# Optimization experiments

Hardware: AMD Instinct MI355X
Metric: run time of the kernel (lower is better)

Reference implementation:

```python
import jax, jax.numpy as jnp
import numpy as np

N = 50000      # nodes in batched graph
E = 800000     # directed edges
F_IN = 64      # node_feature_dim
F_E = 16       # edge_feature_dim
H = 4          # heads
C = 64         # hidden_dim per head
HC = H * C     # 256


def setup_inputs() -> dict:
    key = jax.random.key(0)
    ks = jax.random.split(key, 26)
    rn = lambda k, s, scale=0.1: jax.random.normal(k, s, dtype=jnp.float32) * scale
    inp = {}
    inp["x"] = rn(ks[0], (N, F_IN), 1.0)
    inp["edge_src"] = jax.random.randint(ks[1], (E,), 0, N)
    inp["edge_dst"] = jax.random.randint(ks[2], (E,), 0, N)
    inp["edge_attr"] = rn(ks[3], (E, F_E), 1.0)
    # GATConv layer 1 params
    inp["W1"] = rn(ks[4], (F_IN, HC))
    inp["atts1"] = rn(ks[5], (H, C))
    inp["attd1"] = rn(ks[6], (H, C))
    inp["We1"] = rn(ks[7], (F_E, HC))
    inp["atte1"] = rn(ks[8], (H, C))
    inp["b1"] = jnp.zeros((HC,), jnp.float32)
    inp["g1"] = jnp.ones((HC,), jnp.float32)
    inp["be1"] = jnp.zeros((HC,), jnp.float32)
    # GATConv layer 2 params
    inp["W2"] = rn(ks[9], (HC, HC))
    inp["atts2"] = rn(ks[10], (H, C))
    inp["attd2"] = rn(ks[11], (H, C))
    inp["We2"] = rn(ks[12], (F_E, HC))
    inp["atte2"] = rn(ks[13], (H, C))
    inp["b2"] = jnp.zeros((HC,), jnp.float32)
    inp["g2"] = jnp.ones((HC,), jnp.float32)
    inp["be2"] = jnp.zeros((HC,), jnp.float32)
    # output head
    inp["Wout"] = rn(ks[14], (HC, 1))
    inp["bout"] = jnp.zeros((1,), jnp.float32)
    return inp


def _gat_layer(x, src, dst, eattr, W, att_s, att_d, We, att_e, b):
    """PyG GATConv (concat=True, add_self_loops with fill_value='mean', eval so no dropout)."""
    n = x.shape[0]
    e = src.shape[0]
    # self-loop edge attr = mean of incoming edge attrs per node (0 if none)
    deg = jax.ops.segment_sum(jnp.ones((e,), x.dtype), dst, num_segments=n)
    loop_attr = jax.ops.segment_sum(eattr, dst, num_segments=n) / jnp.maximum(deg, 1.0)[:, None]
    loop = jnp.arange(n)
    src2 = jnp.concatenate([src, loop])
    dst2 = jnp.concatenate([dst, loop])
    ea2 = jnp.concatenate([eattr, loop_attr], axis=0)
    xs = (x @ W).reshape(n, H, C)                          # [N,H,C]
    a_s = jnp.einsum('nhc,hc->nh', xs, att_s)              # [N,H]
    a_d = jnp.einsum('nhc,hc->nh', xs, att_d)
    ee = (ea2 @ We).reshape(-1, H, C)                      # [E+N,H,C]
    a_e = jnp.einsum('ehc,hc->eh', ee, att_e)
    logits = jax.nn.leaky_relu(a_s[src2] + a_d[dst2] + a_e, 0.2)  # [E+N,H]
    m = jax.ops.segment_max(logits, dst2, num_segments=n)
    p = jnp.exp(logits - m[dst2])
    denom = jax.ops.segment_sum(p, dst2, num_segments=n)[dst2] + 1e-16
    alpha = p / denom                                      # segment softmax per dst node
    out = jax.ops.segment_sum(xs[src2] * alpha[:, :, None], dst2, num_segments=n)
    return out.reshape(n, HC) + b


def _bn_relu(x, g, b):
    # BatchNorm1d in training mode (batch statistics), eps=1e-5
    mu = x.mean(axis=0)
    var = ((x - mu) ** 2).mean(axis=0)
    return jax.nn.relu(g * (x - mu) * jax.lax.rsqrt(var + 1e-5) + b)


def reference(x, edge_src, edge_dst, edge_attr,
              W1, atts1, attd1, We1, atte1, b1, g1, be1,
              W2, atts2, attd2, We2, atte2, b2, g2, be2,
              Wout, bout):
    h = _gat_layer(x, edge_src, edge_dst, edge_attr, W1, atts1, attd1, We1, atte1, b1)
    h = _bn_relu(h, g1, be1)
    h = _gat_layer(h, edge_src, edge_dst, edge_attr, W2, atts2, attd2, We2, atte2, b2)
    h = _bn_relu(h, g2, be2)
    return h @ Wout + bout
```

## Files before the change

### kernel.cpp

```cpp
#include <hip/hip_runtime.h>
#include <hip/hip_bf16.h>
#include <stdint.h>

#define NNODES 50000
#define NEDGES 800000
#define HC 256

typedef unsigned short u16;
typedef __attribute__((ext_vector_type(8))) short bf16x8;
typedef __attribute__((ext_vector_type(4))) float f32x4;

__device__ __forceinline__ float b2f(u16 v) {
    return __uint_as_float(((unsigned)v) << 16);
}
__device__ __forceinline__ u16 f2b(float f) {
    unsigned u = __float_as_uint(f);
    u += 0x7fff + ((u >> 16) & 1);
    return (u16)(u >> 16);
}

__device__ __constant__ int dPO[19] = {0,16384,16640,16896,20992,21248,21504,21760,22016,
                                       87552,87808,88064,92160,92416,92672,92928,93184,93440,93441};
static const int hPO[19] = {0,16384,16640,16896,20992,21248,21504,21760,22016,
                            87552,87808,88064,92160,92416,92672,92928,93184,93440,93441};
#define TOTP 93441

__global__ void zero_init(unsigned* __restrict__ p, long nwords) {
    long i = (long)blockIdx.x * blockDim.x + threadIdx.x;
    long stride = (long)gridDim.x * blockDim.x;
    for (; i < nwords; i += stride) p[i] = 0u;
}

__global__ void detect_dtype(const unsigned* __restrict__ xbits, int* __restrict__ flag) {
    __shared__ int cnt;
    if (threadIdx.x == 0) cnt = 0;
    __syncthreads();
    int sane = 0;
    for (int i = threadIdx.x; i < 1024; i += 256) {
        unsigned lo = xbits[i] & 0xffffu;
        int e = (int)((lo >> 7) & 0xff);
        if (e >= 117 && e <= 133) sane++;
    }
    atomicAdd(&cnt, sane);
    __syncthreads();
    if (threadIdx.x == 0) *flag = (cnt >= 512) ? 1 : 0;
}

__global__ void cvt_bf16(const void* __restrict__ src, u16* __restrict__ dst, int n,
                         const int* __restrict__ flag) {
    int isbf16 = *flag;
    long no = (long)n >> 3;
    long i = (long)blockIdx.x * 256 + threadIdx.x;
    long stride = (long)gridDim.x * 256;
    if (isbf16) {
        const uint4* s = (const uint4*)src;
        uint4* d = (uint4*)dst;
        for (; i < no; i += stride) d[i] = s[i];
    } else {
        const float4* s = (const float4*)src;
        uint4* d = (uint4*)dst;
        for (; i < no; i += stride) {
            float4 a = s[i * 2], b = s[i * 2 + 1];
            uint4 o;
            o.x = (unsigned)f2b(a.x) | ((unsigned)f2b(a.y) << 16);
            o.y = (unsigned)f2b(a.z) | ((unsigned)f2b(a.w) << 16);
            o.z = (unsigned)f2b(b.x) | ((unsigned)f2b(b.y) << 16);
            o.w = (unsigned)f2b(b.z) | ((unsigned)f2b(b.w) << 16);
            d[i] = o;
        }
    }
}

struct Ptrs18 { const void* s[18]; };
__global__ void cvt_params(Ptrs18 p, u16* __restrict__ dst, const int* __restrict__ flag) {
    int i = blockIdx.x * 256 + threadIdx.x;
    if (i >= TOTP) return;
    int isbf16 = *flag;
    int idx = 0;
    #pragma unroll
    for (int j = 1; j < 18; j++) idx += (i >= dPO[j]) ? 1 : 0;
    int rel = i - dPO[idx];
    dst[i] = isbf16 ? ((const u16*)p.s[idx])[rel] : f2b(((const float*)p.s[idx])[rel]);
}

__global__ void proj_weight(const u16* __restrict__ W, const u16* __restrict__ att,
                            float* __restrict__ out, int R) {
    int i = blockIdx.x * 256 + threadIdx.x;
    if (i >= R * 4) return;
    int f = i >> 2, h = i & 3;
    float s = 0.f;
    for (int c = 0; c < 64; c++)
        s += b2f(W[f * 256 + h * 64 + c]) * b2f(att[h * 64 + c]);
    out[i] = s;
}

__global__ void proj_weight2(const u16* __restrict__ W, const u16* __restrict__ atta,
                             const u16* __restrict__ attb,
                             float* __restrict__ outa, float* __restrict__ outb, int R) {
    int i = blockIdx.x * 256 + threadIdx.x;
    if (i >= R * 4) return;
    int f = i >> 2, h = i & 3;
    float sa = 0.f, sb = 0.f;
    for (int c = 0; c < 64; c++) {
        float w = b2f(W[f * 256 + h * 64 + c]);
        sa += w * b2f(atta[h * 64 + c]);
        sb += w * b2f(attb[h * 64 + c]);
    }
    outa[i] = sa;
    outb[i] = sb;
}

__global__ void transpose_w(const u16* __restrict__ W, u16* __restrict__ WT, int K) {
    int i = blockIdx.x * 256 + threadIdx.x;
    if (i >= K * 256) return;
    int k = i / 256, c = i % 256;
    WT[c * K + k] = W[i];
}

__global__ void edge_deg(const int* __restrict__ edst, int* __restrict__ deg) {
    int e = blockIdx.x * 256 + threadIdx.x;
    if (e >= NEDGES) return;
    atomicAdd(&deg[edst[e]], 1);
}

__global__ void block_sum(const int* __restrict__ deg, int* __restrict__ bsums, int n) {
    __shared__ int lds[256];
    int i = blockIdx.x * 256 + threadIdx.x;
    lds[threadIdx.x] = (i < n) ? deg[i] : 0;
    __syncthreads();
    for (int s = 128; s; s >>= 1) {
        if (threadIdx.x < s) lds[threadIdx.x] += lds[threadIdx.x + s];
        __syncthreads();
    }
    if (threadIdx.x == 0) bsums[blockIdx.x] = lds[0];
}

__global__ void scan_bsums(const int* __restrict__ bsums, int* __restrict__ boffs, int nb) {
    __shared__ int lds[256];
    int t = threadIdx.x;
    int v = (t < nb) ? bsums[t] : 0;
    lds[t] = v;
    __syncthreads();
    for (int s = 1; s < 256; s <<= 1) {
        int u = (t >= s) ? lds[t - s] : 0;
        __syncthreads();
        lds[t] += u;
        __syncthreads();
    }
    boffs[t] = lds[t] - v;
}

__global__ void write_offsets(const int* __restrict__ deg, const int* __restrict__ boffs,
                              int* __restrict__ off, int* __restrict__ cursor, int n) {
    __shared__ int lds[256];
    int t = threadIdx.x;
    int i = blockIdx.x * 256 + t;
    int v = (i < n) ? deg[i] : 0;
    lds[t] = v;
    __syncthreads();
    for (int s = 1; s < 256; s <<= 1) {
        int u = (t >= s) ? lds[t - s] : 0;
        __syncthreads();
        lds[t] += u;
        __syncthreads();
    }
    int exc = lds[t] - v + boffs[blockIdx.x];
    if (i < n) { off[i] = exc; cursor[i] = exc; }
}

__global__ __launch_bounds__(256) void edge_stage(
    const void* __restrict__ eattr_raw, const int* __restrict__ flag,
    const int* __restrict__ esrc, const int* __restrict__ edst,
    const float* __restrict__ ve1, const float* __restrict__ ve2,
    int* __restrict__ cursor, uint4* __restrict__ rec) {
    int e = blockIdx.x * 256 + threadIdx.x;
    if (e >= NEDGES) return;
    float a[16];
    if (*flag) {
        const u16* s = (const u16*)eattr_raw + (long)e * 16;
        const uint4* q = (const uint4*)s;
        uint4 q0 = q[0], q1 = q[1];
        unsigned w0[8] = {q0.x, q0.y, q0.z, q0.w, q1.x, q1.y, q1.z, q1.w};
        #pragma unroll
        for (int j = 0; j < 8; j++) {
            a[2 * j] = b2f((u16)(w0[j] & 0xffff));
            a[2 * j + 1] = b2f((u16)(w0[j] >> 16));
        }
    } else {
        const float* s = (const float*)eattr_raw + (long)e * 16;
        #pragma unroll
        for (int j = 0; j < 16; j += 4) {
            float4 q = *(const float4*)(s + j);
            a[j] = q.x; a[j + 1] = q.y; a[j + 2] = q.z; a[j + 3] = q.w;
        }
    }
    float s1[4], s2[4];
    #pragma unroll
    for (int h = 0; h < 4; h++) {
        float t1 = 0.f, t2 = 0.f;
        #pragma unroll
        for (int f = 0; f < 16; f++) {
            t1 += a[f] * ve1[f * 4 + h];
            t2 += a[f] * ve2[f * 4 + h];
        }
        s1[h] = t1;
        s2[h] = t2;
    }
    unsigned a1lo = (unsigned)f2b(s1[0]) | ((unsigned)f2b(s1[1]) << 16);
    unsigned a1hi = (unsigned)f2b(s1[2]) | ((unsigned)f2b(s1[3]) << 16);
    unsigned a2lo = (unsigned)f2b(s2[0]) | ((unsigned)f2b(s2[1]) << 16);
    unsigned a2hi = (unsigned)f2b(s2[2]) | ((unsigned)f2b(s2[3]) << 16);
    int d = edst[e];
    int p = atomicAdd(&cursor[d], 1);
    unsigned src = (unsigned)esrc[e];
    rec[(long)p * 2 + 0] = make_uint4(src, a1lo, a1hi, 0u);
    rec[(long)p * 2 + 1] = make_uint4(src, a2lo, a2hi, 0u);
}

__global__ void bn_coef(const float* __restrict__ stats, const u16* __restrict__ g,
                        const u16* __restrict__ be, float* __restrict__ coef) {
    int c = threadIdx.x;
    float mu = stats[c] * (1.0f / NNODES);
    float var = stats[256 + c] * (1.0f / NNODES) - mu * mu;
    var = fmaxf(var, 0.f);
    float rs = rsqrtf(var + 1e-5f);
    float sc = b2f(g[c]) * rs;
    coef[c] = sc;
    coef[256 + c] = b2f(be[c]) - sc * mu;
}

__device__ __forceinline__ void gload_lds16(const u16* g, u16* l) {
    __builtin_amdgcn_global_load_lds(
        (const __attribute__((address_space(1))) unsigned*)g,
        (__attribute__((address_space(3))) unsigned*)l, 16, 0, 0);
}

template <int K, bool BN>
__global__ __launch_bounds__(256) void gemm_tile(const u16* __restrict__ A,
                                                 const u16* __restrict__ WT,
                                                 const float* __restrict__ coef,
                                                 u16* __restrict__ out) {
    __shared__ u16 As[128 * 32];
    __shared__ u16 Bs[128 * 32];
    int tid = threadIdx.x;
    int wave = tid >> 6, lane = tid & 63;
    int wr = wave >> 1, wc = wave & 1;
    int quad = lane >> 4, l15 = lane & 15;
    long row0 = (long)(blockIdx.x >> 1) * 128;
    int col0 = (blockIdx.x & 1) * 128;
    int srow = lane >> 2;
    int soct = (lane & 3) * 8;
    f32x4 acc[4][4] = {};
    for (int kk = 0; kk < K; kk += 32) {
        #pragma unroll
        for (int sub = 0; sub < 2; sub++) {
            int rr = wave * 32 + sub * 16;
            long gr = row0 + rr + srow;
            if (gr >= NNODES) gr = NNODES - 1;
            gload_lds16(A + gr * K + kk + soct, &As[rr * 32]);
            gload_lds16(WT + (long)(col0 + rr + srow) * K + kk + soct, &Bs[rr * 32]);
        }
        __syncthreads();
        bf16x8 av[4], bv[4];
        #pragma unroll
        for (int m = 0; m < 4; m++)
            av[m] = *(const bf16x8*)&As[(wr * 64 + m * 16 + l15) * 32 + quad * 8];
        if (BN) {
            int kb = kk + quad * 8;
            float4 sc0 = *(const float4*)(coef + kb);
            float4 sc1 = *(const float4*)(coef + kb + 4);
            float4 sh0 = *(const float4*)(coef + 256 + kb);
            float4 sh1 = *(const float4*)(coef + 256 + kb + 4);
            float scl[8] = {sc0.x, sc0.y, sc0.z, sc0.w, sc1.x, sc1.y, sc1.z, sc1.w};
            float shf[8] = {sh0.x, sh0.y, sh0.z, sh0.w, sh1.x, sh1.y, sh1.z, sh1.w};
            #pragma unroll
            for (int m = 0; m < 4; m++) {
                #pragma unroll
                for (int j = 0; j < 8; j++) {
                    float v = b2f((u16)av[m][j]);
                    v = fmaxf(v * scl[j] + shf[j], 0.f);
                    av[m][j] = (short)f2b(v);
                }
            }
        }
        #pragma unroll
        for (int n = 0; n < 4; n++)
            bv[n] = *(const bf16x8*)&Bs[(wc * 64 + n * 16 + l15) * 32 + quad * 8];
        #pragma unroll
        for (int m = 0; m < 4; m++)
            #pragma unroll
            for (int n = 0; n < 4; n++)
                acc[m][n] = __builtin_amdgcn_mfma_f32_16x16x32_bf16(av[m], bv[n],
                                                                    acc[m][n], 0, 0, 0);
        __syncthreads();
    }
    #pragma unroll
    for (int m = 0; m < 4; m++) {
        #pragma unroll
        for (int j = 0; j < 4; j++) {
            long r = row0 + wr * 64 + m * 16 + quad * 4 + j;
            if (r < NNODES) {
                u16* op = out + r * HC + col0 + wc * 64 + l15;
                #pragma unroll
                for (int n = 0; n < 4; n++) op[n * 16] = f2b(acc[m][n][j]);
            }
        }
    }
}

template <int K, bool BN>
__global__ __launch_bounds__(256) void proj_att(const u16* __restrict__ X,
                                                const float* __restrict__ coef,
                                                const float* __restrict__ us,
                                                const float* __restrict__ ud,
                                                float* __restrict__ as_, float* __restrict__ ad_) {
    int gw = (blockIdx.x * 256 + threadIdx.x) >> 6;
    int lane = threadIdx.x & 63;
    int node, f0;
    if (K == 64) {
        node = gw * 4 + (lane >> 4);
        f0 = (lane & 15) * 4;
    } else {
        node = gw;
        f0 = lane * 4;
    }
    if (node >= NNODES) return;
    uint2 v = *(const uint2*)(X + (long)node * K + f0);
    float xv[4] = {b2f((u16)(v.x & 0xffffu)), b2f((u16)(v.x >> 16)),
                   b2f((u16)(v.y & 0xffffu)), b2f((u16)(v.y >> 16))};
    float pas[4] = {0.f, 0.f, 0.f, 0.f}, pad[4] = {0.f, 0.f, 0.f, 0.f};
    #pragma unroll
    for (int j = 0; j < 4; j++) {
        int f = f0 + j;
        float x = xv[j];
        if (BN) x = fmaxf(x * coef[f] + coef[256 + f], 0.f);
        #pragma unroll
        for (int h = 0; h < 4; h++) {
            pas[h] += x * us[f * 4 + h];
            pad[h] += x * ud[f * 4 + h];
        }
    }
    const int omax = (K == 64) ? 8 : 32;
    #pragma unroll
    for (int h = 0; h < 4; h++) {
        for (int o = omax; o; o >>= 1) {
            pas[h] += __shfl_xor(pas[h], o);
            pad[h] += __shfl_xor(pad[h], o);
        }
    }
    bool wr = (K == 64) ? ((lane & 15) == 0) : (lane == 0);
    if (wr) {
        #pragma unroll
        for (int h = 0; h < 4; h++) {
            as_[node * 4 + h] = pas[h];
            ad_[node * 4 + h] = pad[h];
        }
    }
}

__global__ __launch_bounds__(256) void gat_fused(
    const u16* __restrict__ xs, const float* __restrict__ as_, const float* __restrict__ ad_,
    const uint4* __restrict__ rec, int layer,
    const int* __restrict__ off, const int* __restrict__ deg,
    const u16* __restrict__ bias, u16* __restrict__ out) {
    __shared__ int s_lds[4][64];
    __shared__ float w_lds[4][64][4];
    int wid = (blockIdx.x * 256 + threadIdx.x) >> 6;
    if (wid >= NNODES) return;
    int wave = threadIdx.x >> 6;
    int lane = threadIdx.x & 63;
    int d = wid;
    int st = off[d], dg = deg[d];
    int slot = lane >> 2, h = lane & 3;
    float adv = ad_[d * 4 + h];
    float m = -1e30f, s = 0.f, sae = 0.f;
    const uint4* rbase = rec + (long)st * 2 + layer;

    if (dg <= 64) {
        for (int i = slot; i < dg; i += 16) {
            uint4 r4 = rbase[(long)i * 2];
            int src = (int)r4.x;
            unsigned wsel = (h & 2) ? r4.z : r4.y;
            float aev = b2f((u16)((h & 1) ? (wsel >> 16) : (wsel & 0xffffu)));
            float t = as_[src * 4 + h] + adv + aev;
            float lg = (t > 0.f) ? t : 0.2f * t;
            if (h == 0) s_lds[wave][i] = src;
            w_lds[wave][i][h] = lg;
            sae += aev;
            float mn = fmaxf(m, lg);
            s = s * __expf(m - mn) + __expf(lg - mn);
            m = mn;
        }
        #pragma unroll
        for (int o = 4; o < 64; o <<= 1) {
            float mo = __shfl_xor(m, o), so = __shfl_xor(s, o), ao = __shfl_xor(sae, o);
            float mn = fmaxf(m, mo);
            s = s * __expf(m - mn) + so * __expf(mo - mn);
            m = mn;
            sae += ao;
        }
        float invs, wself;
        {
            float asv = as_[d * 4 + h];
            float l0 = asv + adv + sae / fmaxf((float)dg, 1.f);
            l0 = (l0 > 0.f) ? l0 : 0.2f * l0;
            float mn = fmaxf(m, l0);
            s = s * __expf(m - mn) + __expf(l0 - mn);
            m = mn;
            invs = 1.f / s;
            wself = __expf(l0 - mn) * invs;
        }
        for (int i = slot; i < dg; i += 16)
            w_lds[wave][i][h] = __expf(w_lds[wave][i][h] - m) * invs;

        int cg = lane & 31, half = lane >> 5;
        int ch8 = cg * 8;
        int h2 = cg >> 3;
        float ws2 = __shfl(wself, h2);
        const u16* xbase = xs + ch8;
        float a0, a1, a2, a3, a4, a5, a6, a7;
        {
            uint4 v = *(const uint4*)(xbase + (long)d * HC);
            float wsf = half ? 0.f : ws2;
            a0 = wsf * b2f((u16)(v.x & 0xffffu)); a1 = wsf * b2f((u16)(v.x >> 16));
            a2 = wsf * b2f((u16)(v.y & 0xffffu)); a3 = wsf * b2f((u16)(v.y >> 16));
            a4 = wsf * b2f((u16)(v.z & 0xffffu)); a5 = wsf * b2f((u16)(v.z >> 16));
            a6 = wsf * b2f((u16)(v.w & 0xffffu)); a7 = wsf * b2f((u16)(v.w >> 16));
        }
        int i = half;
        for (; i + 6 < dg; i += 8) {
            float wA = w_lds[wave][i][h2];     int sA = s_lds[wave][i];
            float wB = w_lds[wave][i + 2][h2]; int sB = s_lds[wave][i + 2];
            float wC = w_lds[wave][i + 4][h2]; int sC = s_lds[wave][i + 4];
            float wD = w_lds[wave][i + 6][h2]; int sD = s_lds[wave][i + 6];
            uint4 vA = *(const uint4*)(xbase + (long)sA * HC);
            uint4 vB = *(const uint4*)(xbase + (long)sB * HC);
            uint4 vC = *(const uint4*)(xbase + (long)sC * HC);
            uint4 vD = *(const uint4*)(xbase + (long)sD * HC);
            a0 += wA * b2f((u16)(vA.x & 0xffffu)) + wB * b2f((u16)(vB.x & 0xffffu))
                + wC * b2f((u16)(vC.x & 0xffffu)) + wD * b2f((u16)(vD.x & 0xffffu));
            a1 += wA * b2f((u16)(vA.x >> 16))     + wB * b2f((u16)(vB.x >> 16))
                + wC * b2f((u16)(vC.x >> 16))     + wD * b2f((u16)(vD.x >> 16));
            a2 += wA * b2f((u16)(vA.y & 0xffffu)) + wB * b2f((u16)(vB.y & 0xffffu))
                + wC * b2f((u16)(vC.y & 0xffffu)) + wD * b2f((u16)(vD.y & 0xffffu));
            a3 += wA * b2f((u16)(vA.y >> 16))     + wB * b2f((u16)(vB.y >> 16))
                + wC * b2f((u16)(vC.y >> 16))     + wD * b2f((u16)(vD.y >> 16));
            a4 += wA * b2f((u16)(vA.z & 0xffffu)) + wB * b2f((u16)(vB.z & 0xffffu))
                + wC * b2f((u16)(vC.z & 0xffffu)) + wD * b2f((u16)(vD.z & 0xffffu));
            a5 += wA * b2f((u16)(vA.z >> 16))     + wB * b2f((u16)(vB.z >> 16))
                + wC * b2f((u16)(vC.z >> 16))     + wD * b2f((u16)(vD.z >> 16));
            a6 += wA * b2f((u16)(vA.w & 0xffffu)) + wB * b2f((u16)(vB.w & 0xffffu))
                + wC * b2f((u16)(vC.w & 0xffffu)) + wD * b2f((u16)(vD.w & 0xffffu));
            a7 += wA * b2f((u16)(vA.w >> 16))     + wB * b2f((u16)(vB.w >> 16))
                + wC * b2f((u16)(vC.w >> 16))     + wD * b2f((u16)(vD.w >> 16));
        }
        for (; i < dg; i += 2) {
            float wA = w_lds[wave][i][h2]; int sA = s_lds[wave][i];
            uint4 vA = *(const uint4*)(xbase + (long)sA * HC);
            a0 += wA * b2f((u16)(vA.x & 0xffffu)); a1 += wA * b2f((u16)(vA.x >> 16));
            a2 += wA * b2f((u16)(vA.y & 0xffffu)); a3 += wA * b2f((u16)(vA.y >> 16));
            a4 += wA * b2f((u16)(vA.z & 0xffffu)); a5 += wA * b2f((u16)(vA.z >> 16));
            a6 += wA * b2f((u16)(vA.w & 0xffffu)); a7 += wA * b2f((u16)(vA.w >> 16));
        }
        a0 += __shfl_xor(a0, 32); a1 += __shfl_xor(a1, 32);
        a2 += __shfl_xor(a2, 32); a3 += __shfl_xor(a3, 32);
        a4 += __shfl_xor(a4, 32); a5 += __shfl_xor(a5, 32);
        a6 += __shfl_xor(a6, 32); a7 += __shfl_xor(a7, 32);
        if (half == 0) {
            uint4 bv = *(const uint4*)(bias + ch8);
            a0 += b2f((u16)(bv.x & 0xffffu)); a1 += b2f((u16)(bv.x >> 16));
            a2 += b2f((u16)(bv.y & 0xffffu)); a3 += b2f((u16)(bv.y >> 16));
            a4 += b2f((u16)(bv.z & 0xffffu)); a5 += b2f((u16)(bv.z >> 16));
            a6 += b2f((u16)(bv.w & 0xffffu)); a7 += b2f((u16)(bv.w >> 16));
            uint4 ov;
            ov.x = (unsigned)f2b(a0) | ((unsigned)f2b(a1) << 16);
            ov.y = (unsigned)f2b(a2) | ((unsigned)f2b(a3) << 16);
            ov.z = (unsigned)f2b(a4) | ((unsigned)f2b(a5) << 16);
            ov.w = (unsigned)f2b(a6) | ((unsigned)f2b(a7) << 16);
            *(uint4*)(out + (long)d * HC + ch8) = ov;
        }
        return;
    }

    for (int base = 0; base < dg; base += 16) {
        int i = base + slot;
        float lg = -1e30f, aev = 0.f, w = 0.f;
        if (i < dg) {
            uint4 r4 = rbase[(long)i * 2];
            int src = (int)r4.x;
            unsigned wsel = (h & 2) ? r4.z : r4.y;
            aev = b2f((u16)((h & 1) ? (wsel >> 16) : (wsel & 0xffffu)));
            float t = as_[src * 4 + h] + adv + aev;
            lg = (t > 0.f) ? t : 0.2f * t;
        }
        sae += aev;
        float mn = fmaxf(m, lg);
        if (i < dg) w = __expf(lg - mn);
        s = s * __expf(m - mn) + w;
        m = mn;
    }
    #pragma unroll
    for (int o = 4; o < 64; o <<= 1) {
        float mo = __shfl_xor(m, o), so = __shfl_xor(s, o), ao = __shfl_xor(sae, o);
        float mn = fmaxf(m, mo);
        s = s * __expf(m - mn) + so * __expf(mo - mn);
        m = mn;
        sae += ao;
    }
    float invs, wself;
    {
        float asv = as_[d * 4 + h];
        float l0 = asv + adv + sae / fmaxf((float)dg, 1.f);
        l0 = (l0 > 0.f) ? l0 : 0.2f * l0;
        float mn = fmaxf(m, l0);
        s = s * __expf(m - mn) + __expf(l0 - mn);
        m = mn;
        invs = 1.f / s;
        wself = __expf(l0 - mn) * invs;
    }
    int h2 = lane >> 4;
    float m2 = __shfl(m, h2);
    float is2 = __shfl(invs, h2);
    float ws2 = __shfl(wself, h2);
    float adv2 = __shfl(adv, h2);
    int cb = lane * 4;
    float a0, a1, a2, a3;
    {
        uint2 v = *(const uint2*)(xs + (long)d * HC + cb);
        a0 = ws2 * b2f((u16)(v.x & 0xffffu)); a1 = ws2 * b2f((u16)(v.x >> 16));
        a2 = ws2 * b2f((u16)(v.y & 0xffffu)); a3 = ws2 * b2f((u16)(v.y >> 16));
    }
    int slot16 = lane & 15;
    int lhi = lane & 48;
    for (int base = 0; base < dg; base += 16) {
        int cnt = min(16, dg - base);
        float wv = 0.f;
        int srcl = 0;
        if (slot16 < cnt) {
            uint4 r4 = rbase[(long)(base + slot16) * 2];
            srcl = (int)r4.x;
            unsigned wsel = (h2 & 2) ? r4.z : r4.y;
            float aev = b2f((u16)((h2 & 1) ? (wsel >> 16) : (wsel & 0xffffu)));
            float t = as_[srcl * 4 + h2] + adv2 + aev;
            t = (t > 0.f) ? t : 0.2f * t;
            wv = __expf(t - m2) * is2;
        }
        for (int j = 0; j < cnt; j++) {
            float w0 = __shfl(wv, lhi | j);
            int s0 = __shfl(srcl, j);
            uint2 v0 = *(const uint2*)(xs + (long)s0 * HC + cb);
            a0 += w0 * b2f((u16)(v0.x & 0xffffu));
            a1 += w0 * b2f((u16)(v0.x >> 16));
            a2 += w0 * b2f((u16)(v0.y & 0xffffu));
            a3 += w0 * b2f((u16)(v0.y >> 16));
        }
    }
    u16 o0 = f2b(a0 + b2f(bias[cb + 0]));
    u16 o1 = f2b(a1 + b2f(bias[cb + 1]));
    u16 o2 = f2b(a2 + b2f(bias[cb + 2]));
    u16 o3 = f2b(a3 + b2f(bias[cb + 3]));
    uint2 ov;
    ov.x = (unsigned)o0 | ((unsigned)o1 << 16);
    ov.y = (unsigned)o2 | ((unsigned)o3 << 16);
    *(uint2*)(out + (long)d * HC + cb) = ov;
}

__global__ __launch_bounds__(256) void bn_stats(const u16* __restrict__ h,
                                                float* __restrict__ stats) {
    __shared__ float lsum[256], lsq[256];
    int t = threadIdx.x;
    int p = t & 127;
    int ro = t >> 7;
    float s0 = 0.f, q0 = 0.f, s1 = 0.f, q1 = 0.f;
    for (int r = blockIdx.x * 2 + ro; r < NNODES; r += gridDim.x * 2) {
        unsigned v = *(const unsigned*)(h + (long)r * HC + 2 * p);
        float lo = b2f((u16)(v & 0xffffu)), hi = b2f((u16)(v >> 16));
        s0 += lo; q0 += lo * lo;
        s1 += hi; q1 += hi * hi;
    }
    if (ro == 1) {
        lsum[2 * p] = s0; lsum[2 * p + 1] = s1;
        lsq[2 * p] = q0;  lsq[2 * p + 1] = q1;
    }
    __syncthreads();
    if (ro == 0) {
        atomicAdd(&stats[2 * p],           s0 + lsum[2 * p]);
        atomicAdd(&stats[2 * p + 1],       s1 + lsum[2 * p + 1]);
        atomicAdd(&stats[256 + 2 * p],     q0 + lsq[2 * p]);
        atomicAdd(&stats[256 + 2 * p + 1], q1 + lsq[2 * p + 1]);
    }
}

__global__ __launch_bounds__(256) void out_head(const u16* __restrict__ h,
                                                const float* __restrict__ coef,
                                                const u16* __restrict__ wout,
                                                const u16* __restrict__ bout,
                                                void* __restrict__ y,
                                                const int* __restrict__ flag) {
    int wid = (blockIdx.x * 256 + threadIdx.x) >> 6;
    int lane = threadIdx.x & 63;
    if (wid >= NNODES) return;
    int c0 = lane * 4;
    uint2 v = *(const uint2*)(h + (long)wid * HC + c0);
    uint2 wv = *(const uint2*)(wout + c0);
    float hv[4] = {b2f((u16)(v.x & 0xffffu)), b2f((u16)(v.x >> 16)),
                   b2f((u16)(v.y & 0xffffu)), b2f((u16)(v.y >> 16))};
    float wf[4] = {b2f((u16)(wv.x & 0xffffu)), b2f((u16)(wv.x >> 16)),
                   b2f((u16)(wv.y & 0xffffu)), b2f((u16)(wv.y >> 16))};
    float p = 0.f;
    #pragma unroll
    for (int j = 0; j < 4; j++) {
        float t = fmaxf(hv[j] * coef[c0 + j] + coef[256 + c0 + j], 0.f);
        p += t * wf[j];
    }
    for (int o = 32; o; o >>= 1) p += __shfl_down(p, o);
    if (lane == 0) {
        float t = p + b2f(bout[0]);
        if (*flag) ((u16*)y)[wid] = f2b(t);
        else       ((float*)y)[wid] = t;
    }
}

extern "C" void kernel_launch(void* const* d_in, const int* in_sizes, int n_in,
                              void* d_out, int out_size, void* d_ws, size_t ws_size,
                              hipStream_t stream) {
    (void)in_sizes; (void)n_in; (void)out_size; (void)ws_size;
    const void* x_raw     = d_in[0];
    const int*  esrc      = (const int*)d_in[1];
    const int*  edst      = (const int*)d_in[2];
    const void* eattr_raw = d_in[3];

    char* ws = (char*)d_ws;
    size_t o = 0;
    auto alloc = [&](size_t bytes) -> char* {
        o = (o + 255) & ~(size_t)255;
        char* p = ws + o;
        o += bytes;
        return p;
    };
    int* dflag = (int*)alloc(256);
    u16* xb   = (u16*)alloc((size_t)NNODES * 64 * 2);
    u16* pall = (u16*)alloc((size_t)TOTP * 2);
    u16 *W1b = pall + hPO[0], *atts1b = pall + hPO[1], *attd1b = pall + hPO[2],
        *We1b = pall + hPO[3], *atte1b = pall + hPO[4], *b1b = pall + hPO[5],
        *g1b = pall + hPO[6], *be1b = pall + hPO[7], *W2b = pall + hPO[8],
        *atts2b = pall + hPO[9], *attd2b = pall + hPO[10], *We2b = pall + hPO[11],
        *atte2b = pall + hPO[12], *b2b = pall + hPO[13], *g2b = pall + hPO[14],
        *be2b = pall + hPO[15], *Woutb = pall + hPO[16], *boutb = pall + hPO[17];
    u16* WT1 = (u16*)alloc(256 * 64 * 2);
    u16* WT2 = (u16*)alloc(256 * 256 * 2);
    float* ve1 = (float*)alloc(64 * 4);
    float* ve2 = (float*)alloc(64 * 4);
    float* us1 = (float*)alloc(256 * 4);
    float* ud1 = (float*)alloc(256 * 4);
    float* us2 = (float*)alloc(1024 * 4);
    float* ud2 = (float*)alloc(1024 * 4);
    float* coef1 = (float*)alloc(512 * 4);
    float* coef2 = (float*)alloc(512 * 4);
    int* deg = (int*)alloc((size_t)NNODES * 4);
    float* stats1 = (float*)alloc(512 * 4);
    float* stats2 = (float*)alloc(512 * 4);
    size_t zero_end = o;
    size_t zero_begin = (size_t)((char*)deg - ws);
    int* off = (int*)alloc((size_t)NNODES * 4);
    int* cursor = (int*)alloc((size_t)NNODES * 4);
    int* bsums = (int*)alloc(256 * 4);
    int* boffs = (int*)alloc(256 * 4);
    uint4* rec = (uint4*)alloc((size_t)NEDGES * 32);
    float* as_ = (float*)alloc((size_t)NNODES * 16);
    float* ad_ = (float*)alloc((size_t)NNODES * 16);
    u16* bufA = (u16*)alloc((size_t)NNODES * HC * 2);
    u16* bufB = (u16*)alloc((size_t)NNODES * HC * 2);

    long zwords = (long)((zero_end - zero_begin) / 4);
    zero_init<<<128, 256, 0, stream>>>((unsigned*)(ws + zero_begin), zwords);
    detect_dtype<<<1, 256, 0, stream>>>((const unsigned*)x_raw, dflag);

    cvt_bf16<<<1024, 256, 0, stream>>>(x_raw, xb, NNODES * 64, dflag);
    Ptrs18 pp;
    for (int i = 0; i < 18; i++) pp.s[i] = d_in[4 + i];
    cvt_params<<<(TOTP + 255) / 256, 256, 0, stream>>>(pp, pall, dflag);

    transpose_w<<<64, 256, 0, stream>>>(W1b, WT1, 64);
    transpose_w<<<256, 256, 0, stream>>>(W2b, WT2, 256);
    proj_weight<<<1, 256, 0, stream>>>(We1b, atte1b, ve1, 16);
    proj_weight<<<1, 256, 0, stream>>>(We2b, atte2b, ve2, 16);
    proj_weight2<<<1, 256, 0, stream>>>(W1b, atts1b, attd1b, us1, ud1, 64);
    proj_weight2<<<4, 256, 0, stream>>>(W2b, atts2b, attd2b, us2, ud2, 256);

    int eblocks = (NEDGES + 255) / 256;
    int nb = (NNODES + 255) / 256;
    edge_deg<<<eblocks, 256, 0, stream>>>(edst, deg);
    block_sum<<<nb, 256, 0, stream>>>(deg, bsums, NNODES);
    scan_bsums<<<1, 256, 0, stream>>>(bsums, boffs, nb);
    write_offsets<<<nb, 256, 0, stream>>>(deg, boffs, off, cursor, NNODES);
    edge_stage<<<eblocks, 256, 0, stream>>>(eattr_raw, dflag, esrc, edst, ve1, ve2,
                                            cursor, rec);

    int gtiles = ((NNODES + 127) / 128) * 2;
    int wblocks = (NNODES * 64 + 255) / 256;
    int pblocks64 = (NNODES + 15) / 16;

    gemm_tile<64, false><<<gtiles, 256, 0, stream>>>(xb, WT1, nullptr, bufA);
    proj_att<64, false><<<pblocks64, 256, 0, stream>>>(xb, nullptr, us1, ud1, as_, ad_);
    gat_fused<<<wblocks, 256, 0, stream>>>(bufA, as_, ad_, rec, 0, off, deg, b1b, bufB);
    bn_stats<<<256, 256, 0, stream>>>(bufB, stats1);
    bn_coef<<<1, 256, 0, stream>>>(stats1, g1b, be1b, coef1);

    gemm_tile<256, true><<<gtiles, 256, 0, stream>>>(bufB, WT2, coef1, bufA);
    proj_att<256, true><<<wblocks, 256, 0, stream>>>(bufB, coef1, us2, ud2, as_, ad_);
    gat_fused<<<wblocks, 256, 0, stream>>>(bufA, as_, ad_, rec, 1, off, deg, b2b, bufB);
    bn_stats<<<256, 256, 0, stream>>>(bufB, stats2);
    bn_coef<<<1, 256, 0, stream>>>(stats2, g2b, be2b, coef2);

    out_head<<<wblocks, 256, 0, stream>>>(bufB, coef2, Woutb, boutb, d_out, dflag);
}
```

Baseline: 542.3 us.

## Merge setup kernels into fewer launches and fold BN coefficient into stats

Several small preparation kernels (zero init, dtype detection, x conversion, param conversion, weight transposes, attention projections, degree counting) are merged into two launches that pick a role per block. The block-offset scan and the offset write become one kernel, with each block redoing the small scan itself. BN coefficients are now computed by the last block to finish bn_stats, detected with an atomic counter, so the separate bn_coef launch goes away. This cuts launch count and the idle gaps between launches, at the cost of a redundant scan in every block and an extra fence and atomic at the end of bn_stats.

Measured after the change: 538.9 us. Within noise of the previous version (-0.6%).

```diff
diff --git a/kernel.cpp b/kernel.cpp
--- a/kernel.cpp
+++ b/kernel.cpp
@@ -17,6 +17,9 @@
     unsigned u = __float_as_uint(f);
     u += 0x7fff + ((u >> 16) & 1);
     return (u16)(u >> 16);
+}
+__device__ __forceinline__ float rdp(const void* p, long i, int bf) {
+    return bf ? b2f(((const u16*)p)[i]) : ((const float*)p)[i];
 }
 
 __device__ __constant__ int dPO[19] = {0,16384,16640,16896,20992,21248,21504,21760,22016,
@@ -25,102 +28,145 @@
                             87552,87808,88064,92160,92416,92672,92928,93184,93440,93441};
 #define TOTP 93441
 
-__global__ void zero_init(unsigned* __restrict__ p, long nwords) {
-    long i = (long)blockIdx.x * blockDim.x + threadIdx.x;
-    long stride = (long)gridDim.x * blockDim.x;
-    for (; i < nwords; i += stride) p[i] = 0u;
-}
-
-__global__ void detect_dtype(const unsigned* __restrict__ xbits, int* __restrict__ flag) {
-    __shared__ int cnt;
-    if (threadIdx.x == 0) cnt = 0;
-    __syncthreads();
-    int sane = 0;
-    for (int i = threadIdx.x; i < 1024; i += 256) {
-        unsigned lo = xbits[i] & 0xffffu;
-        int e = (int)((lo >> 7) & 0xff);
-        if (e >= 117 && e <= 133) sane++;
-    }
-    atomicAdd(&cnt, sane);
-    __syncthreads();
-    if (threadIdx.x == 0) *flag = (cnt >= 512) ? 1 : 0;
-}
-
-__global__ void cvt_bf16(const void* __restrict__ src, u16* __restrict__ dst, int n,
-                         const int* __restrict__ flag) {
-    int isbf16 = *flag;
-    long no = (long)n >> 3;
-    long i = (long)blockIdx.x * 256 + threadIdx.x;
-    long stride = (long)gridDim.x * 256;
-    if (isbf16) {
-        const uint4* s = (const uint4*)src;
-        uint4* d = (uint4*)dst;
-        for (; i < no; i += stride) d[i] = s[i];
+__global__ __launch_bounds__(256) void prep0(unsigned* __restrict__ zp, long nwords,
+                                             const unsigned* __restrict__ xbits,
+                                             int* __restrict__ flag) {
+    if (blockIdx.x < 128) {
+        long i = (long)blockIdx.x * 256 + threadIdx.x;
+        long stride = 128L * 256;
+        for (; i < nwords; i += stride) zp[i] = 0u;
     } else {
-        const float4* s = (const float4*)src;
-        uint4* d = (uint4*)dst;
-        for (; i < no; i += stride) {
-            float4 a = s[i * 2], b = s[i * 2 + 1];
-            uint4 o;
-            o.x = (unsigned)f2b(a.x) | ((unsigned)f2b(a.y) << 16);
-            o.y = (unsigned)f2b(a.z) | ((unsigned)f2b(a.w) << 16);
-            o.z = (unsigned)f2b(b.x) | ((unsigned)f2b(b.y) << 16);
-            o.w = (unsigned)f2b(b.z) | ((unsigned)f2b(b.w) << 16);
-            d[i] = o;
-        }
+        __shared__ int cnt;
+        if (threadIdx.x == 0) cnt = 0;
+        __syncthreads();
+        int sane = 0;
+        for (int i = threadIdx.x; i < 1024; i += 256) {
+            unsigned lo = xbits[i] & 0xffffu;
+            int e = (int)((lo >> 7) & 0xff);
+            if (e >= 117 && e <= 133) sane++;
+        }
+        atomicAdd(&cnt, sane);
+        __syncthreads();
+        if (threadIdx.x == 0) *flag = (cnt >= 512) ? 1 : 0;
     }
 }
 
 struct Ptrs18 { const void* s[18]; };
-__global__ void cvt_params(Ptrs18 p, u16* __restrict__ dst, const int* __restrict__ flag) {
-    int i = blockIdx.x * 256 + threadIdx.x;
-    if (i >= TOTP) return;
-    int isbf16 = *flag;
-    int idx = 0;
-    #pragma unroll
-    for (int j = 1; j < 18; j++) idx += (i >= dPO[j]) ? 1 : 0;
-    int rel = i - dPO[idx];
-    dst[i] = isbf16 ? ((const u16*)p.s[idx])[rel] : f2b(((const float*)p.s[idx])[rel]);
-}
-
-__global__ void proj_weight(const u16* __restrict__ W, const u16* __restrict__ att,
-                            float* __restrict__ out, int R) {
-    int i = blockIdx.x * 256 + threadIdx.x;
-    if (i >= R * 4) return;
-    int f = i >> 2, h = i & 3;
-    float s = 0.f;
-    for (int c = 0; c < 64; c++)
-        s += b2f(W[f * 256 + h * 64 + c]) * b2f(att[h * 64 + c]);
-    out[i] = s;
-}
-
-__global__ void proj_weight2(const u16* __restrict__ W, const u16* __restrict__ atta,
-                             const u16* __restrict__ attb,
-                             float* __restrict__ outa, float* __restrict__ outb, int R) {
-    int i = blockIdx.x * 256 + threadIdx.x;
-    if (i >= R * 4) return;
-    int f = i >> 2, h = i & 3;
-    float sa = 0.f, sb = 0.f;
-    for (int c = 0; c < 64; c++) {
-        float w = b2f(W[f * 256 + h * 64 + c]);
-        sa += w * b2f(atta[h * 64 + c]);
-        sb += w * b2f(attb[h * 64 + c]);
-    }
-    outa[i] = sa;
-    outb[i] = sb;
-}
-
-__global__ void transpose_w(const u16* __restrict__ W, u16* __restrict__ WT, int K) {
-    int i = blockIdx.x * 256 + threadIdx.x;
-    if (i >= K * 256) return;
-    int k = i / 256, c = i % 256;
-    WT[c * K + k] = W[i];
-}
-
-__global__ void edge_deg(const int* __restrict__ edst, int* __restrict__ deg) {
-    int e = blockIdx.x * 256 + threadIdx.x;
-    if (e >= NEDGES) return;
-    atomicAdd(&deg[edst[e]], 1);
+
+#define NB_XB 512
+#define NB_WT1 64
+#define NB_WT2 256
+#define NB_PALL ((TOTP + 255) / 256)
+#define NB_DEG ((NEDGES + 255) / 256)
+#define JB1 (NB_XB)
+#define JB2 (JB1 + NB_WT1)
+#define JB3 (JB2 + NB_WT2)
+#define JB4 (JB3 + NB_PALL)
+#define JB5 (JB4 + 1)
+#define JB6 (JB5 + 1)
+#define JB7 (JB6 + 4)
+#define NB_PREP (JB7 + NB_DEG)
+
+__global__ __launch_bounds__(256) void param_prep(
+    Ptrs18 pp, const void* __restrict__ x_raw, const int* __restrict__ edst,
+    const int* __restrict__ flag,
+    u16* __restrict__ xb, u16* __restrict__ pall,
+    u16* __restrict__ WT1, u16* __restrict__ WT2,
+    float* __restrict__ ve1, float* __restrict__ ve2,
+    float* __restrict__ us1, float* __restrict__ ud1,
+    float* __restrict__ us2, float* __restrict__ ud2,
+    int* __restrict__ deg) {
+    int b = blockIdx.x, t = threadIdx.x;
+    if (b >= JB7) {
+        int e = (b - JB7) * 256 + t;
+        if (e < NEDGES) atomicAdd(&deg[edst[e]], 1);
+        return;
+    }
+    int bf = *flag;
+    if (b < JB1) {
+        long no = (long)NNODES * 64 / 8;
+        long i = (long)b * 256 + t;
+        long stride = (long)NB_XB * 256;
+        if (bf) {
+            const uint4* s = (const uint4*)x_raw;
+            uint4* d = (uint4*)xb;
+            for (; i < no; i += stride) d[i] = s[i];
+        } else {
+            const float4* s = (const float4*)x_raw;
+            uint4* d = (uint4*)xb;
+            for (; i < no; i += stride) {
+                float4 a = s[i * 2], c = s[i * 2 + 1];
+                uint4 o;
+                o.x = (unsigned)f2b(a.x) | ((unsigned)f2b(a.y) << 16);
+                o.y = (unsigned)f2b(a.z) | ((unsigned)f2b(a.w) << 16);
+                o.z = (unsigned)f2b(c.x) | ((unsigned)f2b(c.y) << 16);
+                o.w = (unsigned)f2b(c.z) | ((unsigned)f2b(c.w) << 16);
+                d[i] = o;
+            }
+        }
+        return;
+    }
+    if (b < JB2) {
+        int i = (b - JB1) * 256 + t;
+        int k = i >> 8, c = i & 255;
+        WT1[c * 64 + k] = bf ? ((const u16*)pp.s[0])[i] : f2b(((const float*)pp.s[0])[i]);
+        return;
+    }
+    if (b < JB3) {
+        int i = (b - JB2) * 256 + t;
+        int k = i >> 8, c = i & 255;
+        WT2[c * 256 + k] = bf ? ((const u16*)pp.s[8])[i] : f2b(((const float*)pp.s[8])[i]);
+        return;
+    }
+    if (b < JB4) {
+        int i = (b - JB3) * 256 + t;
+        if (i >= TOTP) return;
+        int idx = 0;
+        #pragma unroll
+        for (int j = 1; j < 18; j++) idx += (i >= dPO[j]) ? 1 : 0;
+        int rel = i - dPO[idx];
+        pall[i] = bf ? ((const u16*)pp.s[idx])[rel] : f2b(((const float*)pp.s[idx])[rel]);
+        return;
+    }
+    if (b < JB5) {
+        if (t < 128) {
+            int i = t & 63;
+            int f = i >> 2, h = i & 3;
+            const void* W = (t < 64) ? pp.s[3] : pp.s[11];
+            const void* A = (t < 64) ? pp.s[4] : pp.s[12];
+            float* o = (t < 64) ? ve1 : ve2;
+            float s = 0.f;
+            for (int c = 0; c < 64; c++)
+                s += rdp(W, f * 256 + h * 64 + c, bf) * rdp(A, h * 64 + c, bf);
+            o[i] = s;
+        }
+        return;
+    }
+    if (b < JB6) {
+        int f = t >> 2, h = t & 3;
+        float sa = 0.f, sb = 0.f;
+        for (int c = 0; c < 64; c++) {
+            float w = rdp(pp.s[0], f * 256 + h * 64 + c, bf);
+            sa += w * rdp(pp.s[1], h * 64 + c, bf);
+            sb += w * rdp(pp.s[2], h * 64 + c, bf);
+        }
+        us1[t] = sa;
+        ud1[t] = sb;
+        return;
+    }
+    {
+        int i = (b - JB6) * 256 + t;
+        if (i >= 1024) return;
+        int f = i >> 2, h = i & 3;
+        float sa = 0.f, sb = 0.f;
+        for (int c = 0; c < 64; c++) {
+            float w = rdp(pp.s[8], f * 256 + h * 64 + c, bf);
+            sa += w * rdp(pp.s[9], h * 64 + c, bf);
+            sb += w * rdp(pp.s[10], h * 64 + c, bf);
+        }
+        us2[i] = sa;
+        ud2[i] = sb;
+    }
 }
 
 __global__ void block_sum(const int* __restrict__ deg, int* __restrict__ bsums, int n) {
@@ -135,11 +181,24 @@
     if (threadIdx.x == 0) bsums[blockIdx.x] = lds[0];
 }
 
-__global__ void scan_bsums(const int* __restrict__ bsums, int* __restrict__ boffs, int nb) {
+__global__ void scan_write(const int* __restrict__ bsums, const int* __restrict__ deg,
+                           int* __restrict__ off, int* __restrict__ cursor, int n, int nb) {
+    __shared__ int sb[256];
     __shared__ int lds[256];
     int t = threadIdx.x;
     int v = (t < nb) ? bsums[t] : 0;
-    lds[t] = v;
+    sb[t] = v;
+    __syncthreads();
+    for (int s = 1; s < 256; s <<= 1) {
+        int u = (t >= s) ? sb[t - s] : 0;
+        __syncthreads();
+        sb[t] += u;
+        __syncthreads();
+    }
+    int boff = sb[blockIdx.x] - bsums[blockIdx.x];
+    int i = blockIdx.x * 256 + t;
+    int dv = (i < n) ? deg[i] : 0;
+    lds[t] = dv;
     __syncthreads();
     for (int s = 1; s < 256; s <<= 1) {
         int u = (t >= s) ? lds[t - s] : 0;
@@ -147,24 +206,7 @@
         lds[t] += u;
         __syncthreads();
     }
-    boffs[t] = lds[t] - v;
-}
-
-__global__ void write_offsets(const int* __restrict__ deg, const int* __restrict__ boffs,
-                              int* __restrict__ off, int* __restrict__ cursor, int n) {
-    __shared__ int lds[256];
-    int t = threadIdx.x;
-    int i = blockIdx.x * 256 + t;
-    int v = (i < n) ? deg[i] : 0;
-    lds[t] = v;
-    __syncthreads();
-    for (int s = 1; s < 256; s <<= 1) {
-        int u = (t >= s) ? lds[t - s] : 0;
-        __syncthreads();
-        lds[t] += u;
-        __syncthreads();
-    }
-    int exc = lds[t] - v + boffs[blockIdx.x];
+    int exc = lds[t] - dv + boff;
     if (i < n) { off[i] = exc; cursor[i] = exc; }
 }
 
@@ -215,18 +257,6 @@
     unsigned src = (unsigned)esrc[e];
     rec[(long)p * 2 + 0] = make_uint4(src, a1lo, a1hi, 0u);
     rec[(long)p * 2 + 1] = make_uint4(src, a2lo, a2hi, 0u);
-}
-
-__global__ void bn_coef(const float* __restrict__ stats, const u16* __restrict__ g,
-                        const u16* __restrict__ be, float* __restrict__ coef) {
-    int c = threadIdx.x;
-    float mu = stats[c] * (1.0f / NNODES);
-    float var = stats[256 + c] * (1.0f / NNODES) - mu * mu;
-    var = fmaxf(var, 0.f);
-    float rs = rsqrtf(var + 1e-5f);
-    float sc = b2f(g[c]) * rs;
-    coef[c] = sc;
-    coef[256 + c] = b2f(be[c]) - sc * mu;
 }
 
 __device__ __forceinline__ void gload_lds16(const u16* g, u16* l) {
@@ -566,8 +596,13 @@
 }
 
 __global__ __launch_bounds__(256) void bn_stats(const u16* __restrict__ h,
-                                                float* __restrict__ stats) {
+                                                float* __restrict__ stats,
+                                                int* __restrict__ cnt,
+                                                const u16* __restrict__ g,
+                                                const u16* __restrict__ be,
+                                                float* __restrict__ coef) {
     __shared__ float lsum[256], lsq[256];
+    __shared__ int last;
     int t = threadIdx.x;
     int p = t & 127;
     int ro = t >> 7;
@@ -588,6 +623,24 @@
         atomicAdd(&stats[2 * p + 1],       s1 + lsum[2 * p + 1]);
         atomicAdd(&stats[256 + 2 * p],     q0 + lsq[2 * p]);
         atomicAdd(&stats[256 + 2 * p + 1], q1 + lsq[2 * p + 1]);
+    }
+    __threadfence();
+    __syncthreads();
+    if (t == 0) {
+        int old = atomicAdd(cnt, 1);
+        last = (old == (int)gridDim.x - 1);
+    }
+    __syncthreads();
+    if (last) {
+        float sum = atomicAdd(&stats[t], 0.f);
+        float sq  = atomicAdd(&stats[256 + t], 0.f);
+        float mu = sum * (1.0f / NNODES);
+        float var = sq * (1.0f / NNODES) - mu * mu;
+        var = fmaxf(var, 0.f);
+        float rs = rsqrtf(var + 1e-5f);
+        float sc = b2f(g[t]) * rs;
+        coef[t] = sc;
+        coef[256 + t] = b2f(be[t]) - sc * mu;
     }
 }
 
@@ -641,12 +694,9 @@
     int* dflag = (int*)alloc(256);
     u16* xb   = (u16*)alloc((size_t)NNODES * 64 * 2);
     u16* pall = (u16*)alloc((size_t)TOTP * 2);
-    u16 *W1b = pall + hPO[0], *atts1b = pall + hPO[1], *attd1b = pall + hPO[2],
-        *We1b = pall + hPO[3], *atte1b = pall + hPO[4], *b1b = pall + hPO[5],
-        *g1b = pall + hPO[6], *be1b = pall + hPO[7], *W2b = pall + hPO[8],
-        *atts2b = pall + hPO[9], *attd2b = pall + hPO[10], *We2b = pall + hPO[11],
-        *atte2b = pall + hPO[12], *b2b = pall + hPO[13], *g2b = pall + hPO[14],
-        *be2b = pall + hPO[15], *Woutb = pall + hPO[16], *boutb = pall + hPO[17];
+    u16 *b1b = pall + hPO[5], *g1b = pall + hPO[6], *be1b = pall + hPO[7],
+        *b2b = pall + hPO[13], *g2b = pall + hPO[14], *be2b = pall + hPO[15],
+        *Woutb = pall + hPO[16], *boutb = pall + hPO[17];
     u16* WT1 = (u16*)alloc(256 * 64 * 2);
     u16* WT2 = (u16*)alloc(256 * 256 * 2);
     float* ve1 = (float*)alloc(64 * 4);
@@ -660,12 +710,13 @@
     int* deg = (int*)alloc((size_t)NNODES * 4);
     float* stats1 = (float*)alloc(512 * 4);
     float* stats2 = (float*)alloc(512 * 4);
+    int* bnc1 = (int*)alloc(256);
+    int* bnc2 = (int*)alloc(256);
     size_t zero_end = o;
     size_t zero_begin = (size_t)((char*)deg - ws);
     int* off = (int*)alloc((size_t)NNODES * 4);
     int* cursor = (int*)alloc((size_t)NNODES * 4);
     int* bsums = (int*)alloc(256 * 4);
-    int* boffs = (int*)alloc(256 * 4);
     uint4* rec = (uint4*)alloc((size_t)NEDGES * 32);
     float* as_ = (float*)alloc((size_t)NNODES * 16);
     float* ad_ = (float*)alloc((size_t)NNODES * 16);
@@ -673,27 +724,18 @@
     u16* bufB = (u16*)alloc((size_t)NNODES * HC * 2);
 
     long zwords = (long)((zero_end - zero_begin) / 4);
-    zero_init<<<128, 256, 0, stream>>>((unsigned*)(ws + zero_begin), zwords);
-    detect_dtype<<<1, 256, 0, stream>>>((const unsigned*)x_raw, dflag);
-
-    cvt_bf16<<<1024, 256, 0, stream>>>(x_raw, xb, NNODES * 64, dflag);
+    prep0<<<129, 256, 0, stream>>>((unsigned*)(ws + zero_begin), zwords,
+                                   (const unsigned*)x_raw, dflag);
+
     Ptrs18 pp;
     for (int i = 0; i < 18; i++) pp.s[i] = d_in[4 + i];
-    cvt_params<<<(TOTP + 255) / 256, 256, 0, stream>>>(pp, pall, dflag);
-
-    transpose_w<<<64, 256, 0, stream>>>(W1b, WT1, 64);
-    transpose_w<<<256, 256, 0, stream>>>(W2b, WT2, 256);
-    proj_weight<<<1, 256, 0, stream>>>(We1b, atte1b, ve1, 16);
-    proj_weight<<<1, 256, 0, stream>>>(We2b, atte2b, ve2, 16);
-    proj_weight2<<<1, 256, 0, stream>>>(W1b, atts1b, attd1b, us1, ud1, 64);
-    proj_weight2<<<4, 256, 0, stream>>>(W2b, atts2b, attd2b, us2, ud2, 256);
+    param_prep<<<NB_PREP, 256, 0, stream>>>(pp, x_raw, edst, dflag, xb, pall, WT1, WT2,
+                                            ve1, ve2, us1, ud1, us2, ud2, deg);
 
     int eblocks = (NEDGES + 255) / 256;
     int nb = (NNODES + 255) / 256;
-    edge_deg<<<eblocks, 256, 0, stream>>>(edst, deg);
     block_sum<<<nb, 256, 0, stream>>>(deg, bsums, NNODES);
-    scan_bsums<<<1, 256, 0, stream>>>(bsums, boffs, nb);
-    write_offsets<<<nb, 256, 0, stream>>>(deg, boffs, off, cursor, NNODES);
+    scan_write<<<nb, 256, 0, stream>>>(bsums, deg, off, cursor, NNODES, nb);
     edge_stage<<<eblocks, 256, 0, stream>>>(eattr_raw, dflag, esrc, edst, ve1, ve2,
                                             cursor, rec);
 
@@ -704,14 +746,12 @@
     gemm_tile<64, false><<<gtiles, 256, 0, stream>>>(xb, WT1, nullptr, bufA);
     proj_att<64, false><<<pblocks64, 256, 0, stream>>>(xb, nullptr, us1, ud1, as_, ad_);
     gat_fused<<<wblocks, 256, 0, stream>>>(bufA, as_, ad_, rec, 0, off, deg, b1b, bufB);
-    bn_stats<<<256, 256, 0, stream>>>(bufB, stats1);
-    bn_coef<<<1, 256, 0, stream>>>(stats1, g1b, be1b, coef1);
+    bn_stats<<<256, 256, 0, stream>>>(bufB, stats1, bnc1, g1b, be1b, coef1);
 
     gemm_tile<256, true><<<gtiles, 256, 0, stream>>>(bufB, WT2, coef1, bufA);
     proj_att<256, true><<<wblocks, 256, 0, stream>>>(bufB, coef1, us2, ud2, as_, ad_);
     gat_fused<<<wblocks, 256, 0, stream>>>(bufA, as_, ad_, rec, 1, off, deg, b2b, bufB);
-    bn_stats<<<256, 256, 0, stream>>>(bufB, stats2);
-    bn_coef<<<1, 256, 0, stream>>>(stats2, g2b, be2b, coef2);
+    bn_stats<<<256, 256, 0, stream>>>(bufB, stats2, bnc2, g2b, be2b, coef2);
 
     out_head<<<wblocks, 256, 0, stream>>>(bufB, coef2, Woutb, boutb, d_out, dflag);
 }
```
